# Kernel optimization log

Hardware: AMD Instinct MI355X
Metric: run time of the kernel (lower is better)

The kernel has to match this reference:

```python
import jax, jax.numpy as jnp
import numpy as np

FOLD_SIZE = 16
FOLDS = 4
LEVELS = 4
LEN_KEEP_LEVEL = 128
SCALE = 8
BASE = jnp.asarray((SCALE ** np.arange(4)[::-1]).astype(np.float32))  # [512,64,8,1]


def setup_inputs() -> dict:
    key = jax.random.key(0)
    x = jax.random.normal(key, (16, 3, 1024, 1024), dtype=jnp.float32)
    return {"x": x}


def _patchify(x):
    B, C, H, W = x.shape
    H -= H % FOLD_SIZE
    W -= W % FOLD_SIZE
    x = x[:, :, :H, :W]
    ph, pw = H // FOLD_SIZE, W // FOLD_SIZE
    p = x.reshape(B, C, ph, FOLD_SIZE, pw, FOLD_SIZE)
    p = p.transpose(0, 2, 4, 1, 3, 5).reshape(B, ph * pw, C, FOLD_SIZE, FOLD_SIZE)
    return p, ph, pw


def _diag_diff(p):
    # |triu(p) - rot90(flip(tril(p), axis=1), -1)| summed over patch dims
    a = jnp.triu(p)
    b = jnp.rot90(jnp.flip(jnp.tril(p), axis=1), -1, axes=(1, 2))
    return jnp.abs(a - b).sum((1, 2))


def _get_direction(patches):
    # patches: [N, fs, fs]
    fs = FOLD_SIZE
    half = fs // 2
    sq_tri = (fs * fs - fs) / 2.0
    sq = fs * fs / 2.0
    d0 = _diag_diff(patches) / sq_tri
    d1 = _diag_diff(jnp.rot90(patches, -1, axes=(1, 2))) / sq_tri
    d2 = jnp.abs(patches[:, :, :half] - patches[:, :, half:]).sum((1, 2)) / sq
    d3 = jnp.abs(patches[:, :half, :] - patches[:, half:, :]).sum((1, 2)) / sq
    directions = jnp.stack([d0, d1, d2, d3], axis=-1)  # [N,4]
    direction = jnp.argmin(directions, axis=-1)
    one_hot = jax.nn.one_hot(direction, 4, dtype=jnp.int32)
    return direction.astype(jnp.int32), one_hot


def _fold(direction, one_hot):
    # 8-neighbor stencil: pad with sentinel 4 (never a valid direction)
    pd = jnp.pad(direction, ((0, 0), (1, 1), (1, 1)), constant_values=4)
    s7, s8, s9 = pd[:, :-2, :-2], pd[:, :-2, 1:-1], pd[:, :-2, 2:]
    s4, s6 = pd[:, 1:-1, :-2], pd[:, 1:-1, 2:]
    s1, s2, s3 = pd[:, 2:, :-2], pd[:, 2:, 1:-1], pd[:, 2:, 2:]
    scope = one_hot.sum(-1)  # computed BEFORE updates, as in the original
    valid = (direction != 4).astype(jnp.int32)
    eq = lambda s: (direction == s).astype(jnp.int32)
    add = jnp.stack([eq(s9) + eq(s1), eq(s7) + eq(s3), eq(s8) + eq(s2), eq(s4) + eq(s6)], axis=-1)
    return one_hot + (scope * valid)[..., None] * add


def reference(x):
    patches, Hp, Wp = _patchify(x)
    B = patches.shape[0]
    p = patches.mean(2).reshape(B * Hp * Wp, FOLD_SIZE, FOLD_SIZE)
    direction, one_hot = _get_direction(p)
    direction = direction.reshape(B, Hp, Wp)
    one_hot = one_hot.reshape(B, Hp, Wp, 4)
    for _ in range(FOLDS):
        one_hot = _fold(direction, one_hot)
    scope = one_hot.sum(-1).reshape(B, Hp * Wp)
    one_hot = one_hot.reshape(B, Hp * Wp, 4)
    # center = flattened argmax of scope; original uses //H and %H (H==W here)
    idx = jnp.argmax(scope, axis=-1)
    center = jnp.stack([idx // Hp, idx % Hp], axis=1)[:, None, :]  # [B,1,2]
    hh, ww = jnp.meshgrid(jnp.arange(Hp), jnp.arange(Wp), indexing='ij')
    cord = jnp.stack([hh, ww], axis=-1).reshape(-1, 2)  # [HW,2]
    distance = ((center - cord[None]) ** 2).sum(-1)  # [B,HW]
    index = jnp.argsort(-distance, axis=-1)  # descending
    oh = jnp.take_along_axis(one_hot, index[..., None], axis=1).astype(jnp.float32)
    token = oh / oh.sum(-1, keepdims=True)
    token = jnp.minimum(jnp.round(token * SCALE), float(SCALE))
    L = token.shape[1]
    token = token[:, : L - L % LEVELS].reshape(B, LEVELS, -1, 4)
    token = (BASE * token).sum(-1).astype(jnp.int32)  # [B,levels,L/levels]
    token = jnp.concatenate([token[:, i, :LEN_KEEP_LEVEL] for i in range(LEVELS)], axis=1)
    return token  # [B, levels*len_keep_level] int tokens
```

## Files before the change

### kernel.cpp

```cpp
#include <hip/hip_runtime.h>
#include <hip/hip_bf16.h>


__global__ __launch_bounds__(256) void k_dir(const float* __restrict__ x,
                                             int* __restrict__ dir,
                                             int* __restrict__ centerkey) {
    int t = threadIdx.x;
    if (blockIdx.x == 0 && t < 16) centerkey[t] = -1;
    int wave = t >> 6, lane = t & 63;
    int P = blockIdx.x * 4 + wave;
    int b = P >> 12, pid = P & 4095;
    int ph = pid >> 6, pw = pid & 63;
    int i = lane >> 2, j0 = (lane & 3) << 2;

    const float* base = x + (size_t)b * 3145728 + (size_t)(ph * 16 + i) * 1024 + pw * 16 + j0;
    float4 a0 = *(const float4*)(base);
    float4 a1 = *(const float4*)(base + 1048576);
    float4 a2 = *(const float4*)(base + 2097152);

    __shared__ float pl[4][16][17];
    float* row = &pl[wave][i][j0];
    row[0] = (a0.x + a1.x + a2.x) / 3.0f;
    row[1] = (a0.y + a1.y + a2.y) / 3.0f;
    row[2] = (a0.z + a1.z + a2.z) / 3.0f;
    row[3] = (a0.w + a1.w + a2.w) / 3.0f;
    __syncthreads();

    const float (*p)[17] = pl[wave];
    double c0 = 0.0, c1 = 0.0, c2 = 0.0, c3 = 0.0;
#pragma unroll
    for (int q = 0; q < 4; ++q) {
        int j = j0 + q;
        float pij = p[i][j];
        if (j > i) {
            c0 += (double)fabsf(pij - p[j][i]);
            c1 += (double)fabsf(p[15 - j][i] - p[15 - i][j]);
        }
        if (j < 8) c2 += (double)fabsf(pij - p[i][j + 8]);
        if (i < 8) c3 += (double)fabsf(pij - p[i + 8][j]);
    }
#pragma unroll
    for (int off = 32; off > 0; off >>= 1) {
        c0 += __shfl_xor(c0, off, 64);
        c1 += __shfl_xor(c1, off, 64);
        c2 += __shfl_xor(c2, off, 64);
        c3 += __shfl_xor(c3, off, 64);
    }
    if (lane == 0) {
        double d0 = c0 / 120.0;
        double d1 = c1 / 120.0;
        double d2 = c2 / 128.0;
        double d3 = c3 / 128.0;
        int dm = 0; double best = d0;
        if (d1 < best) { best = d1; dm = 1; }
        if (d2 < best) { best = d2; dm = 2; }
        if (d3 < best) { best = d3; dm = 3; }
        dir[P] = dm;
    }
}

__global__ __launch_bounds__(256) void k_foldcenter(const int* __restrict__ dir,
                                                    int* __restrict__ oh,
                                                    int* __restrict__ centerkey) {
    int P = blockIdx.x * 256 + threadIdx.x;
    int b = P >> 12, pid = P & 4095;
    int h = pid >> 6, w = pid & 63;
    const int* db = dir + b * 4096;
    int d = db[pid];

    auto get = [&](int hh, int ww) -> int {
        if (hh < 0 || hh > 63 || ww < 0 || ww > 63) return 4;
        return db[hh * 64 + ww];
    };
    int add0 = (get(h - 1, w + 1) == d) + (get(h + 1, w - 1) == d);
    int add1 = (get(h - 1, w - 1) == d) + (get(h + 1, w + 1) == d);
    int add2 = (get(h - 1, w) == d) + (get(h + 1, w) == d);
    int add3 = (get(h, w - 1) == d) + (get(h, w + 1) == d);
    int s = 1 + add0 + add1 + add2 + add3;
    int s2 = s * s;
    int S = 1 + s + s2 + s2 * s;

    ((int4*)oh)[P] = make_int4((d == 0) + add0 * S, (d == 1) + add1 * S,
                               (d == 2) + add2 * S, (d == 3) + add3 * S);

    int key = (s2 * s2 << 12) | (4095 - pid);
#pragma unroll
    for (int off = 32; off > 0; off >>= 1)
        key = max(key, __shfl_xor(key, off, 64));
    __shared__ int wmax[4];
    if ((threadIdx.x & 63) == 0) wmax[threadIdx.x >> 6] = key;
    __syncthreads();
    if (threadIdx.x == 0)
        atomicMax(&centerkey[b], max(max(wmax[0], wmax[1]), max(wmax[2], wmax[3])));
}

__global__ __launch_bounds__(256) void k_token(const int* __restrict__ oh,
                                               const int* __restrict__ centerkey,
                                               int* __restrict__ out) {
    int b = blockIdx.x >> 4;
    int slice = blockIdx.x & 15;
    int t = threadIdx.x;
    int idx = 4095 - (centerkey[b] & 4095);
    int ch = idx >> 6, cw = idx & 63;

    __shared__ int keys[4096];
#pragma unroll
    for (int q = 0; q < 16; ++q) {
        int j = q * 256 + t;
        int dh = ch - (j >> 6), dw = cw - (j & 63);
        keys[j] = ((8191 - (dh * dh + dw * dw)) << 12) | j;
    }
    __syncthreads();

    int k = slice * 256 + t;
    int dh = ch - (k >> 6), dw = cw - (k & 63);
    int mykey = ((8191 - (dh * dh + dw * dw)) << 12) | k;

    int r0 = 0, r1 = 0, r2 = 0, r3 = 0;
    const int4* k4 = (const int4*)keys;
#pragma unroll 8
    for (int j = 0; j < 1024; ++j) {
        int4 v = k4[j];
        r0 += (v.x < mykey);
        r1 += (v.y < mykey);
        r2 += (v.z < mykey);
        r3 += (v.w < mykey);
    }
    int rank = (r0 + r1) + (r2 + r3);

    int level = rank >> 10, pil = rank & 1023;
    if (pil < 128) {
        int4 o = ((const int4*)oh)[b * 4096 + k];
        float sum = (float)(o.x + o.y + o.z + o.w);
        float t0 = fminf(rintf(((float)o.x / sum) * 8.0f), 8.0f);
        float t1 = fminf(rintf(((float)o.y / sum) * 8.0f), 8.0f);
        float t2 = fminf(rintf(((float)o.z / sum) * 8.0f), 8.0f);
        float t3 = fminf(rintf(((float)o.w / sum) * 8.0f), 8.0f);
        float tok = 512.0f * t0 + 64.0f * t1 + 8.0f * t2 + t3;
        out[b * 512 + (level << 7) + pil] = (int)tok;
    }
}

extern "C" void kernel_launch(void* const* d_in, const int* in_sizes, int n_in,
                              void* d_out, int out_size, void* d_ws, size_t ws_size,
                              hipStream_t stream) {
    const float* x = (const float*)d_in[0];
    int* out = (int*)d_out;

    char* ws = (char*)d_ws;
    int* dir       = (int*)(ws);
    int* oh        = (int*)(ws + (256 << 10));
    int* centerkey = (int*)(ws + (256 << 10) + (1 << 20));

    k_dir       <<<16384, 256, 0, stream>>>(x, dir, centerkey);
    k_foldcenter<<<256,   256, 0, stream>>>(dir, oh, centerkey);
    k_token     <<<256,   256, 0, stream>>>(oh, centerkey, out);
}
```

Baseline: 301.0 us.

## Coalesce patch loads across row tiles and compute distance rank analytically

k_dir now has each block load full 256-wide row strips (16 patches) with contiguous float4 reads per wave into a shared tile, then evaluate four patches per wave. This replaces the earlier pattern where each wave read one 16x16 patch in short 64-byte row segments. k_token drops the 4096-element shared-memory pairwise rank count and instead counts, per row, how many cells lie closer to the center using an integer square root, with explicit handling of ties. This removes O(N) comparisons per thread but adds sqrt logic whose boundary and tie cases must be exact.

```diff
diff --git a/kernel.cpp b/kernel.cpp
--- a/kernel.cpp
+++ b/kernel.cpp
@@ -8,54 +8,64 @@
     int t = threadIdx.x;
     if (blockIdx.x == 0 && t < 16) centerkey[t] = -1;
     int wave = t >> 6, lane = t & 63;
-    int P = blockIdx.x * 4 + wave;
-    int b = P >> 12, pid = P & 4095;
-    int ph = pid >> 6, pw = pid & 63;
-    int i = lane >> 2, j0 = (lane & 3) << 2;
+    int b    = blockIdx.x >> 8;
+    int rem  = blockIdx.x & 255;
+    int ph   = rem >> 2;
+    int tile = rem & 3;
 
-    const float* base = x + (size_t)b * 3145728 + (size_t)(ph * 16 + i) * 1024 + pw * 16 + j0;
-    float4 a0 = *(const float4*)(base);
-    float4 a1 = *(const float4*)(base + 1048576);
-    float4 a2 = *(const float4*)(base + 2097152);
+    __shared__ float mean[16][257];
 
-    __shared__ float pl[4][16][17];
-    float* row = &pl[wave][i][j0];
-    row[0] = (a0.x + a1.x + a2.x) / 3.0f;
-    row[1] = (a0.y + a1.y + a2.y) / 3.0f;
-    row[2] = (a0.z + a1.z + a2.z) / 3.0f;
-    row[3] = (a0.w + a1.w + a2.w) / 3.0f;
+    const float* bx = x + (size_t)b * 3145728 + (size_t)(ph * 16) * 1024 + tile * 256 + lane * 4;
+#pragma unroll
+    for (int rr = 0; rr < 4; ++rr) {
+        int r = wave * 4 + rr;
+        const float* rp = bx + (size_t)r * 1024;
+        float4 a0 = *(const float4*)(rp);
+        float4 a1 = *(const float4*)(rp + 1048576);
+        float4 a2 = *(const float4*)(rp + 2097152);
+        float* m = &mean[r][lane * 4];
+        m[0] = (a0.x + a1.x + a2.x) / 3.0f;
+        m[1] = (a0.y + a1.y + a2.y) / 3.0f;
+        m[2] = (a0.z + a1.z + a2.z) / 3.0f;
+        m[3] = (a0.w + a1.w + a2.w) / 3.0f;
+    }
     __syncthreads();
 
-    const float (*p)[17] = pl[wave];
-    double c0 = 0.0, c1 = 0.0, c2 = 0.0, c3 = 0.0;
+    int i = lane >> 2, j0 = (lane & 3) << 2;
 #pragma unroll
-    for (int q = 0; q < 4; ++q) {
-        int j = j0 + q;
-        float pij = p[i][j];
-        if (j > i) {
-            c0 += (double)fabsf(pij - p[j][i]);
-            c1 += (double)fabsf(p[15 - j][i] - p[15 - i][j]);
+    for (int pp = 0; pp < 4; ++pp) {
+        int pat = wave * 4 + pp;
+        int cb = pat * 16;
+        double c0 = 0.0, c1 = 0.0, c2 = 0.0, c3 = 0.0;
+#pragma unroll
+        for (int q = 0; q < 4; ++q) {
+            int j = j0 + q;
+            float pij = mean[i][cb + j];
+            if (j > i) {
+                c0 += (double)fabsf(pij - mean[j][cb + i]);
+                c1 += (double)fabsf(mean[15 - j][cb + i] - mean[15 - i][cb + j]);
+            }
+            if (j < 8) c2 += (double)fabsf(pij - mean[i][cb + j + 8]);
+            if (i < 8) c3 += (double)fabsf(pij - mean[i + 8][cb + j]);
         }
-        if (j < 8) c2 += (double)fabsf(pij - p[i][j + 8]);
-        if (i < 8) c3 += (double)fabsf(pij - p[i + 8][j]);
-    }
 #pragma unroll
-    for (int off = 32; off > 0; off >>= 1) {
-        c0 += __shfl_xor(c0, off, 64);
-        c1 += __shfl_xor(c1, off, 64);
-        c2 += __shfl_xor(c2, off, 64);
-        c3 += __shfl_xor(c3, off, 64);
-    }
-    if (lane == 0) {
-        double d0 = c0 / 120.0;
-        double d1 = c1 / 120.0;
-        double d2 = c2 / 128.0;
-        double d3 = c3 / 128.0;
-        int dm = 0; double best = d0;
-        if (d1 < best) { best = d1; dm = 1; }
-        if (d2 < best) { best = d2; dm = 2; }
-        if (d3 < best) { best = d3; dm = 3; }
-        dir[P] = dm;
+        for (int off = 32; off > 0; off >>= 1) {
+            c0 += __shfl_xor(c0, off, 64);
+            c1 += __shfl_xor(c1, off, 64);
+            c2 += __shfl_xor(c2, off, 64);
+            c3 += __shfl_xor(c3, off, 64);
+        }
+        if (lane == 0) {
+            double d0 = c0 / 120.0;
+            double d1 = c1 / 120.0;
+            double d2 = c2 / 128.0;
+            double d3 = c3 / 128.0;
+            int dm = 0; double best = d0;
+            if (d1 < best) { best = d1; dm = 1; }
+            if (d2 < best) { best = d2; dm = 2; }
+            if (d3 < best) { best = d3; dm = 3; }
+            dir[b * 4096 + ph * 64 + tile * 16 + pat] = dm;
+        }
     }
 }
 
@@ -98,35 +108,31 @@
                                                const int* __restrict__ centerkey,
                                                int* __restrict__ out) {
     int b = blockIdx.x >> 4;
-    int slice = blockIdx.x & 15;
-    int t = threadIdx.x;
+    int k = (blockIdx.x & 15) * 256 + threadIdx.x;
     int idx = 4095 - (centerkey[b] & 4095);
     int ch = idx >> 6, cw = idx & 63;
+    int hp = k >> 6, wp = k & 63;
+    int dhp = ch - hp, dwp = cw - wp;
+    int dp = dhp * dhp + dwp * dwp;
 
-    __shared__ int keys[4096];
-#pragma unroll
-    for (int q = 0; q < 16; ++q) {
-        int j = q * 256 + t;
-        int dh = ch - (j >> 6), dw = cw - (j & 63);
-        keys[j] = ((8191 - (dh * dh + dw * dw)) << 12) | j;
+    int rank = 0;
+#pragma unroll 4
+    for (int h = 0; h < 64; ++h) {
+        int dh = ch - h;
+        int tt = dp - dh * dh;
+        if (tt < 0) { rank += 64; continue; }
+        int s = (int)sqrtf((float)tt);
+        if (s * s > tt) --s;
+        else if ((s + 1) * (s + 1) <= tt) ++s;
+        int lo = max(0, cw - s), hi = min(63, cw + s);
+        rank += 64 - (hi - lo + 1);
+        if (s * s == tt) {
+            int base = h << 6;
+            int w1 = cw - s, w2 = cw + s;
+            if (w1 >= 0 && w1 <= 63 && (base + w1) < k) ++rank;
+            if (s > 0 && w2 >= 0 && w2 <= 63 && (base + w2) < k) ++rank;
+        }
     }
-    __syncthreads();
-
-    int k = slice * 256 + t;
-    int dh = ch - (k >> 6), dw = cw - (k & 63);
-    int mykey = ((8191 - (dh * dh + dw * dw)) << 12) | k;
-
-    int r0 = 0, r1 = 0, r2 = 0, r3 = 0;
-    const int4* k4 = (const int4*)keys;
-#pragma unroll 8
-    for (int j = 0; j < 1024; ++j) {
-        int4 v = k4[j];
-        r0 += (v.x < mykey);
-        r1 += (v.y < mykey);
-        r2 += (v.z < mykey);
-        r3 += (v.w < mykey);
-    }
-    int rank = (r0 + r1) + (r2 + r3);
 
     int level = rank >> 10, pil = rank & 1023;
     if (pil < 128) {
@@ -152,7 +158,7 @@
     int* oh        = (int*)(ws + (256 << 10));
     int* centerkey = (int*)(ws + (256 << 10) + (1 << 20));
 
-    k_dir       <<<16384, 256, 0, stream>>>(x, dir, centerkey);
-    k_foldcenter<<<256,   256, 0, stream>>>(dir, oh, centerkey);
-    k_token     <<<256,   256, 0, stream>>>(oh, centerkey, out);
+    k_dir       <<<4096, 256, 0, stream>>>(x, dir, centerkey);
+    k_foldcenter<<<256,  256, 0, stream>>>(dir, oh, centerkey);
+    k_token     <<<256,  256, 0, stream>>>(oh, centerkey, out);
 }
```

Result: faster. 293.7 us (-2.4%).
